# Performance work log

Measured on AMD Instinct MI355X. Metric: run time of the kernel, lower is better.

The kernel has to match this reference:

```python
import jax, jax.numpy as jnp
import numpy as np

N = 300000
GRID = 256
K = 27  # 3x3x3 kernel offsets
C = 128


def _build_neighbors(rng):
    # sample unique occupied voxels in a GRID^3 lattice (sorted linear ids)
    lin = np.unique(rng.integers(0, GRID ** 3, size=int(N * 1.3)))[:N]
    z = lin // (GRID * GRID)
    y = (lin // GRID) % GRID
    x = lin % GRID
    nbr = np.full((N, K), -1, np.int32)
    k = 0
    for dz in (-1, 0, 1):
        for dy in (-1, 0, 1):
            for dx in (-1, 0, 1):
                nz, ny, nx = z + dz, y + dy, x + dx
                valid = (nz >= 0) & (nz < GRID) & (ny >= 0) & (ny < GRID) & (nx >= 0) & (nx < GRID)
                nlin = (nz * GRID + ny) * GRID + nx
                pos = np.clip(np.searchsorted(lin, nlin), 0, N - 1)
                found = valid & (lin[pos] == nlin)
                nbr[:, k] = np.where(found, pos, -1).astype(np.int32)
                k += 1
    return nbr


def setup_inputs() -> dict:
    key = jax.random.key(0)
    ks = jax.random.split(key, 8)
    s = 0.05
    rng = np.random.default_rng(0)
    nbr_idx = jnp.asarray(_build_neighbors(rng))
    return {
        "x_feat": jnp.ones((N, 1), jnp.float32),
        "W_in": jax.random.normal(ks[0], (K, 1, C), jnp.float32) * s,
        "b_in": jnp.zeros((C,), jnp.float32),
        "W_res": jax.random.normal(ks[1], (3, 2, K, C, C), jnp.float32) * s,
        "b_res": jnp.zeros((3, 2, C), jnp.float32),
        "W_out": jax.random.normal(ks[2], (K, C, C), jnp.float32) * s,
        "b_out": jnp.zeros((C,), jnp.float32),
        "Wf1": jax.random.normal(ks[3], (C, C), jnp.float32) * s,
        "bf1": jnp.zeros((C,), jnp.float32),
        "Wf2": jax.random.normal(ks[4], (C, C), jnp.float32) * s,
        "bf2": jnp.zeros((C,), jnp.float32),
        "Wf3": jax.random.normal(ks[5], (C, 3), jnp.float32) * s,
        "bf3": jnp.zeros((3,), jnp.float32),
        "nbr_idx": nbr_idx,
    }


def _sconv(x, nbr, W, b):
    # sparse 3^3 conv: per-offset gather -> GEMM -> masked accumulate
    # x: [N,Cin], nbr: [N,K] (-1 = no neighbor), W: [K,Cin,Cout]
    Cout = W.shape[-1]
    def body(k, acc):
        idx = nbr[:, k]
        g = jnp.where((idx >= 0)[:, None], x[jnp.maximum(idx, 0)], 0.0)
        return acc + g @ W[k]
    acc = jnp.zeros((x.shape[0], Cout), x.dtype)
    return jax.lax.fori_loop(0, W.shape[0], body, acc) + b


def _decoder(x_feat, nbr, W_in, b_in, W_res, b_res, W_out, b_out, Wf1, bf1, Wf2, bf2, Wf3, bf3):
    h = jax.nn.relu(_sconv(x_feat, nbr, W_in, b_in))
    for i in range(W_res.shape[0]):  # ResNetBlock: conv-relu-conv + residual
        r = jax.nn.relu(_sconv(h, nbr, W_res[i, 0], b_res[i, 0]))
        r = _sconv(r, nbr, W_res[i, 1], b_res[i, 1])
        h = h + r
    h = _sconv(h, nbr, W_out, b_out)
    # fc stack of 1x1 convs (pointwise GEMMs)
    h = jax.nn.relu(h @ Wf1 + bf1)
    h = jax.nn.relu(h @ Wf2 + bf2)
    return h @ Wf3 + bf3  # [N,3] predicted coordinate offsets


def reference(x_feat, W_in, b_in, W_res, b_res, W_out, b_out, Wf1, bf1, Wf2, bf2, Wf3, bf3, nbr_idx):
    return _decoder(x_feat, nbr_idx, W_in, b_in, W_res, b_res, W_out, b_out, Wf1, bf1, Wf2, bf2, Wf3, bf3)
```

## Files before the change

kernel.cpp:

```cpp
#include <hip/hip_runtime.h>
#include <hip/hip_bf16.h>
#include <stdint.h>

#define NNODES 300000
#define KNBR   27
#define CDIM   128
#define P_ROWS   219968
#define MAXTILES 2048
#define MAXSLOT  16
#define NT_SELF  ((NNODES + 127) / 128)
#define TPB      4


typedef __bf16 bf16x8_t __attribute__((ext_vector_type(8)));
typedef __bf16 bf16x4_t __attribute__((ext_vector_type(4)));
typedef float  f32x4_t  __attribute__((ext_vector_type(4)));

union BP8 { bf16x8_t v; __hip_bfloat16 h[8]; };
union BP4 { bf16x4_t v; __hip_bfloat16 h[4]; };

__device__ __forceinline__ void gl2lds16(const void* g, void* l) {
  __builtin_amdgcn_global_load_lds(
      reinterpret_cast<const __attribute__((address_space(1))) uint32_t*>(
          reinterpret_cast<uintptr_t>(g)),
      reinterpret_cast<__attribute__((address_space(3))) uint32_t*>(
          reinterpret_cast<uintptr_t>(l)),
      16, 0, 0);
}

__global__ void prep_weights(const float* __restrict__ Wres,
                             const float* __restrict__ Wout,
                             const float* __restrict__ Wf1,
                             const float* __restrict__ Wf2,
                             __hip_bfloat16* __restrict__ wbf) {
  int b = blockIdx.x;
  int m = b >> 7;
  int cout = b & 127;
  int cin = threadIdx.x;
  const float* src;
  if (m < 162)      src = Wres + (size_t)m * 16384;
  else if (m < 189) src = Wout + (size_t)(m - 162) * 16384;
  else if (m == 189) src = Wf1;
  else               src = Wf2;
  float v = src[cin * 128 + cout];
  int sp = (cin & 15) * 8 + (cin >> 4);
  wbf[(size_t)m * 16384 + cout * 128 + sp] = __float2bfloat16(v);
}

__global__ void prep_bias(const float* __restrict__ b_res,
                          const float* __restrict__ b_out,
                          const float* __restrict__ bf1,
                          const float* __restrict__ bf2,
                          float* __restrict__ bp) {
  int v = blockIdx.x;
  int p = threadIdx.x;
  const float* src;
  if (v < 6)       src = b_res + v * 128;
  else if (v == 6) src = b_out;
  else if (v == 7) src = bf1;
  else             src = bf2;
  bp[v * 128 + p] = src[(p & 7) * 16 + (p >> 3)];
}

__global__ void prep_win(const float* __restrict__ Win,
                         __hip_bfloat16* __restrict__ WinT) {
  int c = threadIdx.x;
  for (int k = 0; k < 32; ++k)
    WinT[c * 32 + k] = __float2bfloat16(k < 27 ? Win[k * 128 + c] : 0.0f);
}

__global__ void init_meta(int* __restrict__ segcnt, __hip_bfloat16* __restrict__ z) {
  int t = threadIdx.x;
  if (t < 32) segcnt[t] = 0;
  if (t == 0) { segcnt[128] = 0; segcnt[129] = 0; }
  z[t] = __float2bfloat16(0.0f);
}

__global__ void count_pairs(const int* __restrict__ nbr, int* __restrict__ segcnt,
                            unsigned int* __restrict__ nmask,
                            int* __restrict__ vlist) {
  __shared__ int lc[27];
  int t = threadIdx.x;
  if (t < 27) lc[t] = 0;
  __syncthreads();
  int n = blockIdx.x * 256 + t;
  if (n < NNODES) {
    int nb[27];
    #pragma unroll
    for (int k = 0; k < 27; ++k) nb[k] = nbr[n * 27 + k];
    unsigned int mask = 0;
    #pragma unroll
    for (int k = 0; k < 27; ++k)
      if (k != 13 && nb[k] >= 0) mask |= (1u << k);
    int pc = __popc(mask);
    while (pc > MAXSLOT) {
      mask &= ~(1u << (31 - __clz((int)mask)));
      --pc;
    }
    unsigned int m = mask;
    int j = 0;
    while (m) {
      int k = __ffs(m) - 1; m &= m - 1;
      vlist[n * MAXSLOT + j] = nb[k]; ++j;
      atomicAdd(&lc[k], 1);
    }
    nmask[n] = mask;
  }
  __syncthreads();
  if (t < 27 && t != 13 && lc[t]) atomicAdd(&segcnt[t], lc[t]);
}

__global__ void scan_tiles(const int* __restrict__ segcnt,
                           int* __restrict__ segbase, int* __restrict__ seglen,
                           int* __restrict__ cursor,
                           int* __restrict__ tile_k, int* __restrict__ tile_row0,
                           int* __restrict__ tile_rows,
                           int* __restrict__ ntile) {
  __shared__ int sbase[27], slen[27], tbase[27];
  int t = threadIdx.x;
  for (int i = t; i < MAXTILES; i += 256) tile_k[i] = -1;
  if (t < 32) cursor[t] = 0;
  if (t == 0) {
    int base = 0, tb = 0;
    for (int k = 0; k < 27; ++k) {
      int c = (k == 13) ? 0 : segcnt[k];
      if (base + c > P_ROWS) c = P_ROWS - base;
      if (c < 0) c = 0;
      sbase[k] = base; slen[k] = c; tbase[k] = tb;
      base += c;
      tb += (c + 127) >> 7;
    }
    ntile[0] = tb;
  }
  __syncthreads();
  if (t < 27) {
    segbase[t] = sbase[t];
    seglen[t] = slen[t];
    if (t != 13) {
      int idx = tbase[t];
      for (int r = 0; r < slen[t]; r += 128, ++idx) {
        if (idx < MAXTILES) {
          tile_k[idx] = t;
          tile_row0[idx] = sbase[t] + r;
          tile_rows[idx] = (slen[t] - r < 128) ? (slen[t] - r) : 128;
        }
      }
    }
  }
}

__global__ void fill_pairs(const unsigned int* __restrict__ nmask,
                           const int* __restrict__ vlist,
                           const int* __restrict__ segbase, const int* __restrict__ seglen,
                           int* __restrict__ cursor,
                           int* __restrict__ pr_src, int* __restrict__ pr_dst,
                           int* __restrict__ dinfo, int* __restrict__ dcursor) {
  __shared__ int lc[27], lb[27];
  __shared__ int dloc, dbase_s;
  int t = threadIdx.x;
  if (t < 27) lc[t] = 0;
  if (t == 0) dloc = 0;
  __syncthreads();
  int n = blockIdx.x * 256 + t;
  unsigned int mask = (n < NNODES) ? nmask[n] : 0u;
  int myj = __popc(mask);
  int myoff = myj ? atomicAdd(&dloc, myj) : 0;
  unsigned int m = mask;
  while (m) { int k = __ffs(m) - 1; m &= m - 1; atomicAdd(&lc[k], 1); }
  __syncthreads();
  if (t < 27) { lb[t] = lc[t] ? atomicAdd(&cursor[t], lc[t]) : 0; lc[t] = 0; }
  if (t == 0) dbase_s = dloc ? atomicAdd(dcursor, dloc) : 0;
  __syncthreads();
  if (n < NNODES) {
    int dbase = dbase_s + myoff;
    int jj = 0, vidx = 0;
    m = mask;
    while (m) {
      int k = __ffs(m) - 1; m &= m - 1;
      int lp = atomicAdd(&lc[k], 1);
      int pos = lb[k] + lp;
      if (pos < seglen[k]) {
        int slot = segbase[k] + pos;
        pr_src[slot] = vlist[n * MAXSLOT + vidx];
        pr_dst[slot] = dbase + jj;
        ++jj;
      }
      ++vidx;
    }
    dinfo[n] = (dbase << 5) | jj;
  }
}

__global__ void build_g(const float* __restrict__ xf, const int* __restrict__ nbr,
                        __hip_bfloat16* __restrict__ G) {
  int e = blockIdx.x * 256 + threadIdx.x;
  if (e >= NNODES * 32) return;
  int n = e >> 5, j = e & 31;
  float v = 0.0f;
  if (j < 27) {
    int idx = nbr[n * 27 + j];
    if (idx >= 0) v = xf[idx];
  }
  G[e] = __float2bfloat16(v);
}

__global__ __launch_bounds__(256, 2)
void l1_gemm(const __hip_bfloat16* __restrict__ G,
             const __hip_bfloat16* __restrict__ WinT,
             const float* __restrict__ bin,
             __hip_bfloat16* __restrict__ Aout) {
  __shared__ unsigned short As[128 * 32];

  const int t    = threadIdx.x;
  const int wid  = t >> 6;
  const int lane = t & 63;
  const int quad = lane >> 4;
  const int l16  = lane & 15;
  const int m0   = blockIdx.x * 128;
  const int m_base = (wid & 1) * 64;
  const int n_base = (wid >> 1) * 64;

  bf16x8_t bfr[4];
  #pragma unroll
  for (int ni = 0; ni < 4; ++ni)
    bfr[ni] = *(const bf16x8_t*)(WinT + (n_base + ni * 16 + l16) * 32 + quad * 8);

  float bv[4];
  #pragma unroll
  for (int ni = 0; ni < 4; ++ni) bv[ni] = bin[n_base + ni * 16 + l16];

  const char* Gb = (const char*)(G + (size_t)m0 * 32);
  #pragma unroll
  for (int i = 0; i < 2; ++i) {
    int row = i * 64 + (t >> 2);
    int slot = t & 3;
    gl2lds16(Gb + (size_t)row * 64 + ((slot ^ (row & 3)) * 16),
             (char*)As + i * 4096 + t * 16);
  }
  __syncthreads();

  f32x4_t acc[4][4];
  #pragma unroll
  for (int i = 0; i < 4; ++i)
    #pragma unroll
    for (int j = 0; j < 4; ++j)
      acc[i][j] = (f32x4_t){0.f, 0.f, 0.f, 0.f};

  bf16x8_t af[4];
  #pragma unroll
  for (int mi = 0; mi < 4; ++mi)
    af[mi] = *(const bf16x8_t*)(As + (m_base + mi * 16 + l16) * 32 +
                                ((quad ^ (l16 & 3)) * 8));
  #pragma unroll
  for (int mi = 0; mi < 4; ++mi)
    #pragma unroll
    for (int ni = 0; ni < 4; ++ni)
      acc[mi][ni] = __builtin_amdgcn_mfma_f32_16x16x32_bf16(af[mi], bfr[ni], acc[mi][ni], 0, 0, 0);

  const int nb4 = n_base >> 4;
  #pragma unroll
  for (int mi = 0; mi < 4; ++mi)
    #pragma unroll
    for (int r = 0; r < 4; ++r) {
      int node = m0 + m_base + mi * 16 + quad * 4 + r;
      if (node < NNODES) {
        BP4 o;
        #pragma unroll
        for (int ni = 0; ni < 4; ++ni) {
          float v = acc[mi][ni][r] + bv[ni];
          v = v > 0.0f ? v : 0.0f;
          o.h[ni] = __float2bfloat16(v);
        }
        *(bf16x4_t*)(Aout + (size_t)node * 128 + l16 * 8 + nb4) = o.v;
      }
    }
}

__global__ __launch_bounds__(256, 2)
void pair_gemm(const __hip_bfloat16* __restrict__ Ain,
               const __hip_bfloat16* __restrict__ Wl,
               const int* __restrict__ pr_src,
               const int* __restrict__ pr_dst,
               const int* __restrict__ tile_k, const int* __restrict__ tile_row0,
               const int* __restrict__ tile_rows,
               __hip_bfloat16* __restrict__ P,
               const __hip_bfloat16* __restrict__ zrow) {
  const int t    = threadIdx.x;
  const int wid  = t >> 6;
  const int lane = t & 63;
  const int quad = lane >> 4;
  const int l16  = lane & 15;
  const int m_base = wid * 32;

  bf16x8_t bfr[8][4];
  int tk_cur = -1;

  #pragma unroll 1
  for (int it = 0; it < TPB; ++it) {
    const int tile = blockIdx.x * TPB + it;
    if (tile >= MAXTILES) break;
    const int tk = tile_k[tile];
    if (tk < 0) break;
    const int row0 = tile_row0[tile];
    const int rows = tile_rows[tile];

    if (tk != tk_cur) {
      const __hip_bfloat16* Wb = Wl + (size_t)tk * 16384;
      #pragma unroll
      for (int ni = 0; ni < 8; ++ni)
        #pragma unroll
        for (int kk = 0; kk < 4; ++kk)
          bfr[ni][kk] = *(const bf16x8_t*)(Wb + (ni * 16 + l16) * 128 + kk * 32 + quad * 8);
      tk_cur = tk;
    }

    const __hip_bfloat16* rp[2];
    #pragma unroll
    for (int mi = 0; mi < 2; ++mi) {
      int row = m_base + mi * 16 + l16;
      rp[mi] = zrow;
      if (row < rows) rp[mi] = Ain + (size_t)pr_src[row0 + row] * 128;
    }
    int dst[2][4];
    #pragma unroll
    for (int mi = 0; mi < 2; ++mi)
      #pragma unroll
      for (int r = 0; r < 4; ++r) {
        int row = m_base + mi * 16 + quad * 4 + r;
        dst[mi][r] = (row < rows) ? pr_dst[row0 + row] : -1;
      }

    f32x4_t acc[2][8];
    #pragma unroll
    for (int i = 0; i < 2; ++i)
      #pragma unroll
      for (int j = 0; j < 8; ++j)
        acc[i][j] = (f32x4_t){0.f, 0.f, 0.f, 0.f};

    #pragma unroll
    for (int kk = 0; kk < 4; ++kk) {
      bf16x8_t af[2];
      #pragma unroll
      for (int mi = 0; mi < 2; ++mi)
        af[mi] = *(const bf16x8_t*)(rp[mi] + kk * 32 + quad * 8);
      #pragma unroll
      for (int mi = 0; mi < 2; ++mi)
        #pragma unroll
        for (int ni = 0; ni < 8; ++ni)
          acc[mi][ni] = __builtin_amdgcn_mfma_f32_16x16x32_bf16(af[mi], bfr[ni][kk], acc[mi][ni], 0, 0, 0);
    }

    #pragma unroll
    for (int mi = 0; mi < 2; ++mi)
      #pragma unroll
      for (int r = 0; r < 4; ++r) {
        if (dst[mi][r] >= 0) {
          BP8 o;
          #pragma unroll
          for (int ni = 0; ni < 8; ++ni)
            o.h[ni] = __float2bfloat16(acc[mi][ni][r]);
          *(bf16x8_t*)(P + (size_t)dst[mi][r] * 128 + l16 * 8) = o.v;
        }
      }
  }
}

template <int EPI, bool HASP>
__global__ __launch_bounds__(256, 2)
void self_gemm(const __hip_bfloat16* __restrict__ Ain,
               const __hip_bfloat16* __restrict__ W13,
               const float* __restrict__ bp,
               const __hip_bfloat16* __restrict__ P,
               const int* __restrict__ dinfo,
               __hip_bfloat16* __restrict__ Aout,
               const __hip_bfloat16* __restrict__ zrow) {
  const int t    = threadIdx.x;
  const int wid  = t >> 6;
  const int lane = t & 63;
  const int quad = lane >> 4;
  const int l16  = lane & 15;
  const int m_base = wid * 32;

  bf16x8_t bfr[8][4];
  #pragma unroll
  for (int ni = 0; ni < 8; ++ni)
    #pragma unroll
    for (int kk = 0; kk < 4; ++kk)
      bfr[ni][kk] = *(const bf16x8_t*)(W13 + (ni * 16 + l16) * 128 + kk * 32 + quad * 8);

  float bb[8];
  {
    f32x4_t b0 = *(const f32x4_t*)(bp + l16 * 8);
    f32x4_t b1 = *(const f32x4_t*)(bp + l16 * 8 + 4);
    #pragma unroll
    for (int i = 0; i < 4; ++i) { bb[i] = b0[i]; bb[i + 4] = b1[i]; }
  }

  #pragma unroll 1
  for (int tile = blockIdx.x; tile < NT_SELF; tile += gridDim.x) {
    const int m0 = tile * 128;

    int dif[2][4];
    if (HASP) {
      #pragma unroll
      for (int mi = 0; mi < 2; ++mi)
        #pragma unroll
        for (int r = 0; r < 4; ++r) {
          int node = m0 + m_base + mi * 16 + quad * 4 + r;
          dif[mi][r] = (node < NNODES) ? dinfo[node] : 0;
        }
    }

    f32x4_t acc[2][8];
    #pragma unroll
    for (int i = 0; i < 2; ++i)
      #pragma unroll
      for (int j = 0; j < 8; ++j)
        acc[i][j] = (f32x4_t){0.f, 0.f, 0.f, 0.f};

    const __hip_bfloat16* Abase = Ain + (size_t)(m0 + m_base + l16) * 128;

    #pragma unroll
    for (int kk = 0; kk < 4; ++kk) {
      bf16x8_t af[2];
      #pragma unroll
      for (int mi = 0; mi < 2; ++mi)
        af[mi] = *(const bf16x8_t*)(Abase + mi * 2048 + kk * 32 + quad * 8);
      #pragma unroll
      for (int mi = 0; mi < 2; ++mi)
        #pragma unroll
        for (int ni = 0; ni < 8; ++ni)
          acc[mi][ni] = __builtin_amdgcn_mfma_f32_16x16x32_bf16(af[mi], bfr[ni][kk], acc[mi][ni], 0, 0, 0);
    }

    #pragma unroll
    for (int mi = 0; mi < 2; ++mi) {
      const int nodeb = m0 + m_base + mi * 16 + quad * 4;
      bf16x8_t hold[4], pf[4];
      int cnt4[4], base4[4];
      #pragma unroll
      for (int r = 0; r < 4; ++r) {
        int node = nodeb + r;
        bool ok = node < NNODES;
        if (EPI == 1)
          hold[r] = *(const bf16x8_t*)((ok ? Aout + (size_t)node * 128 : zrow) + l16 * 8);
        if (HASP) {
          int d = dif[mi][r];
          cnt4[r] = d & 31;
          base4[r] = d >> 5;
          pf[r] = *(const bf16x8_t*)((cnt4[r] > 0 ? P + (size_t)base4[r] * 128 : zrow) + l16 * 8);
        }
      }
      #pragma unroll
      for (int r = 0; r < 4; ++r) {
        int node = nodeb + r;
        if (node >= NNODES) continue;
        float add[8];
        #pragma unroll
        for (int ni = 0; ni < 8; ++ni) add[ni] = bb[ni];
        if (HASP) {
          if (cnt4[r] > 0) {
            #pragma unroll
            for (int ni = 0; ni < 8; ++ni) add[ni] += (float)pf[r][ni];
          }
          for (int j = 1; j < cnt4[r]; ++j) {
            bf16x8_t pv = *(const bf16x8_t*)(P + (size_t)(base4[r] + j) * 128 + l16 * 8);
            #pragma unroll
            for (int ni = 0; ni < 8; ++ni) add[ni] += (float)pv[ni];
          }
        }
        BP8 o;
        #pragma unroll
        for (int ni = 0; ni < 8; ++ni) {
          float v = acc[mi][ni][r] + add[ni];
          if (EPI == 0) {
            v = v > 0.0f ? v : 0.0f;
            o.h[ni] = __float2bfloat16(v);
          } else if (EPI == 1) {
            o.h[ni] = __float2bfloat16((float)hold[r][ni] + v);
          } else {
            o.h[ni] = __float2bfloat16(v);
          }
        }
        *(bf16x8_t*)(Aout + (size_t)node * 128 + l16 * 8) = o.v;
      }
    }
  }
}

__global__ void layer1_kernel(const float* __restrict__ xf,
                              const float* __restrict__ Win,
                              const float* __restrict__ bin,
                              const int* __restrict__ nbr,
                              __hip_bfloat16* __restrict__ abf) {
  int n = blockIdx.x;
  int c = threadIdx.x;
  float acc = bin[c];
  #pragma unroll 9
  for (int k = 0; k < KNBR; ++k) {
    int idx = nbr[n * KNBR + k];
    if (idx >= 0) acc += xf[idx] * Win[k * 128 + c];
  }
  acc = acc > 0.0f ? acc : 0.0f;
  int sp = (c & 15) * 8 + (c >> 4);
  abf[(size_t)n * 128 + sp] = __float2bfloat16(acc);
}

template <int EPI>
__global__ __launch_bounds__(256, 2)
void sconv_kernel(const __hip_bfloat16* __restrict__ Ain,
                  const __hip_bfloat16* __restrict__ Wt,
                  const float* __restrict__ bias,
                  const int* __restrict__ nbr,
                  int nk,
                  __hip_bfloat16* __restrict__ Aout,
                  const __hip_bfloat16* __restrict__ zrow) {
  __shared__ unsigned short As[128 * 128];
  __shared__ unsigned short Bs[128 * 128];

  const int t    = threadIdx.x;
  const int wid  = t >> 6;
  const int lane = t & 63;
  const int quad = lane >> 4;
  const int l16  = lane & 15;
  const int m0   = blockIdx.x * 128;

  f32x4_t acc[4][4];
  #pragma unroll
  for (int i = 0; i < 4; ++i)
    #pragma unroll
    for (int j = 0; j < 4; ++j)
      acc[i][j] = (f32x4_t){0.f, 0.f, 0.f, 0.f};

  const int m_base = (wid & 1) * 64;
  const int n_base = (wid >> 1) * 64;

  for (int k = 0; k < nk; ++k) {
    {
      const char* wsrc = (const char*)(Wt + (size_t)k * 16384);
      #pragma unroll
      for (int i = 0; i < 8; ++i) {
        uint32_t off = (uint32_t)wid * 8192 + (uint32_t)i * 1024;
        int row = wid * 32 + i * 4 + quad;
        uint32_t goff = (uint32_t)row * 256 + (uint32_t)((l16 ^ (row & 7)) * 16);
        gl2lds16(wsrc + goff, (char*)Bs + off);
      }
    }
    {
      #pragma unroll
      for (int i = 0; i < 8; ++i) {
        int r = i * 16 + wid * 4 + quad;
        int node = m0 + r;
        const __hip_bfloat16* rowp;
        if (nbr) {
          int idx = (node < NNODES) ? nbr[node * KNBR + k] : -1;
          rowp = (idx >= 0) ? (Ain + (size_t)idx * 128) : zrow;
        } else {
          rowp = (node < NNODES) ? (Ain + (size_t)node * 128) : zrow;
        }
        uint32_t ldsoff = (uint32_t)(i * 16 + wid * 4) * 256;
        gl2lds16((const char*)rowp + ((l16 ^ (r & 7)) * 16), (char*)As + ldsoff);
      }
    }
    __syncthreads();

    #pragma unroll
    for (int kk = 0; kk < 4; ++kk) {
      const int p = ((kk * 4 + quad) ^ (l16 & 7)) * 8;
      bf16x8_t af[4], bfr[4];
      #pragma unroll
      for (int mi = 0; mi < 4; ++mi)
        af[mi] = *(const bf16x8_t*)(As + (m_base + mi * 16 + l16) * 128 + p);
      #pragma unroll
      for (int ni = 0; ni < 4; ++ni)
        bfr[ni] = *(const bf16x8_t*)(Bs + (n_base + ni * 16 + l16) * 128 + p);
      #pragma unroll
      for (int mi = 0; mi < 4; ++mi)
        #pragma unroll
        for (int ni = 0; ni < 4; ++ni)
          acc[mi][ni] = __builtin_amdgcn_mfma_f32_16x16x32_bf16(af[mi], bfr[ni], acc[mi][ni], 0, 0, 0);
    }
    __syncthreads();
  }

  const int nb4 = n_base >> 4;
  #pragma unroll
  for (int ni = 0; ni < 4; ++ni) {
    int sp = l16 * 8 + nb4 + ni;
    float bvv = bias[sp];
    #pragma unroll
    for (int mi = 0; mi < 4; ++mi) {
      #pragma unroll
      for (int r = 0; r < 4; ++r) {
        int row = m_base + mi * 16 + quad * 4 + r;
        int node = m0 + row;
        if (node < NNODES) {
          float v = acc[mi][ni][r] + bvv;
          size_t o = (size_t)node * 128 + sp;
          if (EPI == 0) {
            v = v > 0.0f ? v : 0.0f;
            Aout[o] = __float2bfloat16(v);
          } else if (EPI == 1) {
            Aout[o] = __float2bfloat16(__bfloat162float(Aout[o]) + v);
          } else {
            Aout[o] = __float2bfloat16(v);
          }
        }
      }
    }
  }
}

__global__ void fc3_kernel(const __hip_bfloat16* __restrict__ r,
                           const float* __restrict__ W,
                           const float* __restrict__ b,
                           float* __restrict__ out) {
  int n = blockIdx.x * 256 + threadIdx.x;
  if (n >= NNODES) return;
  float a0 = b[0], a1 = b[1], a2 = b[2];
  const bf16x8_t* rp = (const bf16x8_t*)(r + (size_t)n * 128);
  #pragma unroll
  for (int c8 = 0; c8 < 16; ++c8) {
    bf16x8_t v8 = rp[c8];
    #pragma unroll
    for (int j = 0; j < 8; ++j) {
      float v = (float)v8[j];
      int c = j * 16 + c8;
      a0 += v * W[c * 3 + 0];
      a1 += v * W[c * 3 + 1];
      a2 += v * W[c * 3 + 2];
    }
  }
  out[n * 3 + 0] = a0;
  out[n * 3 + 1] = a1;
  out[n * 3 + 2] = a2;
}

extern "C" void kernel_launch(void* const* d_in, const int* in_sizes, int n_in,
                              void* d_out, int out_size, void* d_ws, size_t ws_size,
                              hipStream_t stream) {
  const float* x_feat = (const float*)d_in[0];
  const float* W_in   = (const float*)d_in[1];
  const float* b_in   = (const float*)d_in[2];
  const float* W_res  = (const float*)d_in[3];
  const float* b_res  = (const float*)d_in[4];
  const float* W_out  = (const float*)d_in[5];
  const float* b_out  = (const float*)d_in[6];
  const float* Wf1    = (const float*)d_in[7];
  const float* bf1    = (const float*)d_in[8];
  const float* Wf2    = (const float*)d_in[9];
  const float* bf2    = (const float*)d_in[10];
  const float* Wf3    = (const float*)d_in[11];
  const float* bf3    = (const float*)d_in[12];
  const int*   nbr    = (const int*)d_in[13];
  float* out = (float*)d_out;

  char* ws = (char*)d_ws;
  __hip_bfloat16* abf0 = (__hip_bfloat16*)ws;
  __hip_bfloat16* abf1 = (__hip_bfloat16*)(ws +  76800000);
  __hip_bfloat16* wbf  = (__hip_bfloat16*)(ws + 153600000);
  __hip_bfloat16* zrow = (__hip_bfloat16*)(ws + 159858688);
  __hip_bfloat16* P    = (__hip_bfloat16*)(ws + 159858944);
  __hip_bfloat16* WinT = (__hip_bfloat16*)(ws + 159858944 + 56320000 - 8192);
  int* pr_dst    = (int*)(ws + 216178944);
  unsigned int* nmask = (unsigned int*)(ws + 217058944);
  int* dinfo     = (int*)(ws + 235378944);
  int* pr_src    = (int*)(ws + 236578944);
  int* segcnt    = (int*)(ws + 237458944);
  int* segbase   = segcnt + 32;
  int* seglen    = segcnt + 64;
  int* cursor    = segcnt + 96;
  int* ntile     = segcnt + 128;
  int* dcursor   = segcnt + 129;
  int* tile_k    = (int*)(ws + 237463040);
  int* tile_row0 = tile_k + MAXTILES;
  int* tile_rows = tile_k + 2 * MAXTILES;
  float* bp      = (float*)(ws + 237487616);
  __hip_bfloat16* G = abf1;
  int* vlist = (int*)P;
  const size_t SPARSE_NEED = 237487616 + 4608 + 512;

  const int GB = (NNODES + 127) / 128;
  __hip_bfloat16* W0 = wbf;

  prep_weights<<<191 * 128, 128, 0, stream>>>(W_res, W_out, Wf1, Wf2, wbf);
  init_meta<<<1, 128, 0, stream>>>(segcnt, zrow);

  if (ws_size >= SPARSE_NEED) {
    prep_bias<<<9, 128, 0, stream>>>(b_res, b_out, bf1, bf2, bp);
    prep_win<<<1, 128, 0, stream>>>(W_in, WinT);
    build_g<<<(NNODES * 32 + 255) / 256, 256, 0, stream>>>(x_feat, nbr, G);
    l1_gemm<<<GB, 256, 0, stream>>>(G, WinT, b_in, abf0);

    const int CB2 = (NNODES + 255) / 256;
    count_pairs<<<CB2, 256, 0, stream>>>(nbr, segcnt, nmask, vlist);
    scan_tiles<<<1, 256, 0, stream>>>(segcnt, segbase, seglen, cursor,
                                      tile_k, tile_row0, tile_rows, ntile);
    fill_pairs<<<CB2, 256, 0, stream>>>(nmask, vlist, segbase, seglen, cursor,
                                        pr_src, pr_dst, dinfo, dcursor);

    #define CONV(IN, OUT, WLAYER, BV, EPI)                                             \
      pair_gemm<<<MAXTILES / TPB, 256, 0, stream>>>(IN, WLAYER, pr_src, pr_dst,        \
                                                    tile_k, tile_row0, tile_rows,      \
                                                    P, zrow);                          \
      self_gemm<EPI, true><<<512, 256, 0, stream>>>(IN, (WLAYER) + 13 * 16384,         \
                                                    bp + (BV) * 128, P, dinfo, OUT, zrow);

    CONV(abf0, abf1, W0 +   0 * 16384, 0, 0)
    CONV(abf1, abf0, W0 +  27 * 16384, 1, 1)
    CONV(abf0, abf1, W0 +  54 * 16384, 2, 0)
    CONV(abf1, abf0, W0 +  81 * 16384, 3, 1)
    CONV(abf0, abf1, W0 + 108 * 16384, 4, 0)
    CONV(abf1, abf0, W0 + 135 * 16384, 5, 1)
    CONV(abf0, abf1, W0 + 162 * 16384, 6, 2)
    #undef CONV

    self_gemm<0, false><<<512, 256, 0, stream>>>(abf1, W0 + 189 * 16384, bp + 7 * 128,
                                                 nullptr, nullptr, abf0, zrow);
    self_gemm<0, false><<<512, 256, 0, stream>>>(abf0, W0 + 190 * 16384, bp + 8 * 128,
                                                 nullptr, nullptr, abf1, zrow);
  } else {
    prep_bias<<<9, 128, 0, stream>>>(b_res, b_out, bf1, bf2, bp);
    layer1_kernel<<<NNODES, 128, 0, stream>>>(x_feat, W_in, b_in, nbr, abf0);
    sconv_kernel<0><<<GB, 256, 0, stream>>>(abf0, W0 +   0 * 16384, bp + 0 * 128, nbr, 27, abf1, zrow);
    sconv_kernel<1><<<GB, 256, 0, stream>>>(abf1, W0 +  27 * 16384, bp + 1 * 128, nbr, 27, abf0, zrow);
    sconv_kernel<0><<<GB, 256, 0, stream>>>(abf0, W0 +  54 * 16384, bp + 2 * 128, nbr, 27, abf1, zrow);
    sconv_kernel<1><<<GB, 256, 0, stream>>>(abf1, W0 +  81 * 16384, bp + 3 * 128, nbr, 27, abf0, zrow);
    sconv_kernel<0><<<GB, 256, 0, stream>>>(abf0, W0 + 108 * 16384, bp + 4 * 128, nbr, 27, abf1, zrow);
    sconv_kernel<1><<<GB, 256, 0, stream>>>(abf1, W0 + 135 * 16384, bp + 5 * 128, nbr, 27, abf0, zrow);
    sconv_kernel<2><<<GB, 256, 0, stream>>>(abf0, W0 + 162 * 16384, bp + 6 * 128, nbr, 27, abf1, zrow);
    sconv_kernel<0><<<GB, 256, 0, stream>>>(abf1, W0 + 189 * 16384, bp + 7 * 128, nullptr, 1, abf0, zrow);
    sconv_kernel<0><<<GB, 256, 0, stream>>>(abf0, W0 + 190 * 16384, bp + 8 * 128, nullptr, 1, abf1, zrow);
  }

  fc3_kernel<<<(NNODES + 255) / 256, 256, 0, stream>>>(abf1, Wf3, bf3, out);
}
```

Measured before the change: 973.5 us.

## Stage conv weights in swizzled LDS instead of registers to raise occupancy

Both pair_gemm and self_gemm now load the 128x128 bf16 weight tile into LDS with async global-to-LDS copies, using an XOR swizzle, and read B fragments from LDS per k-step instead of holding 128 VGPRs of weights. This frees registers so launch bounds can rise from 2 to 4 blocks per CU. pair_gemm drops its multi-tile-per-block loop and launches one block per tile, and the self_gemm grid doubles. The trade is extra LDS traffic per MFMA plus a full weight reload for every tile, which loses the previous reuse across consecutive tiles with the same offset.

```diff
diff --git a/kernel.cpp b/kernel.cpp
--- a/kernel.cpp
+++ b/kernel.cpp
@@ -9,7 +9,7 @@
 #define MAXTILES 2048
 #define MAXSLOT  16
 #define NT_SELF  ((NNODES + 127) / 128)
-#define TPB      4
+#define SELF_GRID 1024
 
 
 typedef __bf16 bf16x8_t __attribute__((ext_vector_type(8)));
@@ -276,7 +276,7 @@
     }
 }
 
-__global__ __launch_bounds__(256, 2)
+__global__ __launch_bounds__(256, 4)
 void pair_gemm(const __hip_bfloat16* __restrict__ Ain,
                const __hip_bfloat16* __restrict__ Wl,
                const int* __restrict__ pr_src,
@@ -285,6 +285,13 @@
                const int* __restrict__ tile_rows,
                __hip_bfloat16* __restrict__ P,
                const __hip_bfloat16* __restrict__ zrow) {
+  __shared__ unsigned short Ws[128 * 128];
+
+  const int tk = tile_k[blockIdx.x];
+  if (tk < 0) return;
+  const int row0 = tile_row0[blockIdx.x];
+  const int rows = tile_rows[blockIdx.x];
+
   const int t    = threadIdx.x;
   const int wid  = t >> 6;
   const int lane = t & 63;
@@ -292,81 +299,73 @@
   const int l16  = lane & 15;
   const int m_base = wid * 32;
 
-  bf16x8_t bfr[8][4];
-  int tk_cur = -1;
-
-  #pragma unroll 1
-  for (int it = 0; it < TPB; ++it) {
-    const int tile = blockIdx.x * TPB + it;
-    if (tile >= MAXTILES) break;
-    const int tk = tile_k[tile];
-    if (tk < 0) break;
-    const int row0 = tile_row0[tile];
-    const int rows = tile_rows[tile];
-
-    if (tk != tk_cur) {
-      const __hip_bfloat16* Wb = Wl + (size_t)tk * 16384;
-      #pragma unroll
-      for (int ni = 0; ni < 8; ++ni)
-        #pragma unroll
-        for (int kk = 0; kk < 4; ++kk)
-          bfr[ni][kk] = *(const bf16x8_t*)(Wb + (ni * 16 + l16) * 128 + kk * 32 + quad * 8);
-      tk_cur = tk;
-    }
-
-    const __hip_bfloat16* rp[2];
-    #pragma unroll
-    for (int mi = 0; mi < 2; ++mi) {
-      int row = m_base + mi * 16 + l16;
-      rp[mi] = zrow;
-      if (row < rows) rp[mi] = Ain + (size_t)pr_src[row0 + row] * 128;
-    }
-    int dst[2][4];
+  {
+    const char* wsrc = (const char*)(Wl + (size_t)tk * 16384);
+    #pragma unroll
+    for (int i = 0; i < 8; ++i) {
+      int row = wid * 32 + i * 4 + quad;
+      gl2lds16(wsrc + (uint32_t)row * 256 + (uint32_t)((l16 ^ (row & 7)) * 16),
+               (char*)Ws + wid * 8192 + i * 1024 + lane * 16);
+    }
+  }
+
+  const __hip_bfloat16* rp[2];
+  #pragma unroll
+  for (int mi = 0; mi < 2; ++mi) {
+    int row = m_base + mi * 16 + l16;
+    rp[mi] = zrow;
+    if (row < rows) rp[mi] = Ain + (size_t)pr_src[row0 + row] * 128;
+  }
+  int dst[2][4];
+  #pragma unroll
+  for (int mi = 0; mi < 2; ++mi)
+    #pragma unroll
+    for (int r = 0; r < 4; ++r) {
+      int row = m_base + mi * 16 + quad * 4 + r;
+      dst[mi][r] = (row < rows) ? pr_dst[row0 + row] : -1;
+    }
+
+  __syncthreads();
+
+  f32x4_t acc[2][8];
+  #pragma unroll
+  for (int i = 0; i < 2; ++i)
+    #pragma unroll
+    for (int j = 0; j < 8; ++j)
+      acc[i][j] = (f32x4_t){0.f, 0.f, 0.f, 0.f};
+
+  #pragma unroll
+  for (int kk = 0; kk < 4; ++kk) {
+    bf16x8_t af[2];
     #pragma unroll
     for (int mi = 0; mi < 2; ++mi)
-      #pragma unroll
-      for (int r = 0; r < 4; ++r) {
-        int row = m_base + mi * 16 + quad * 4 + r;
-        dst[mi][r] = (row < rows) ? pr_dst[row0 + row] : -1;
-      }
-
-    f32x4_t acc[2][8];
-    #pragma unroll
-    for (int i = 0; i < 2; ++i)
-      #pragma unroll
-      for (int j = 0; j < 8; ++j)
-        acc[i][j] = (f32x4_t){0.f, 0.f, 0.f, 0.f};
-
-    #pragma unroll
-    for (int kk = 0; kk < 4; ++kk) {
-      bf16x8_t af[2];
+      af[mi] = *(const bf16x8_t*)(rp[mi] + kk * 32 + quad * 8);
+    #pragma unroll
+    for (int ni = 0; ni < 8; ++ni) {
+      bf16x8_t bw = *(const bf16x8_t*)(Ws + (ni * 16 + l16) * 128 +
+                                       (((kk * 4 + quad) ^ (l16 & 7)) * 8));
       #pragma unroll
       for (int mi = 0; mi < 2; ++mi)
-        af[mi] = *(const bf16x8_t*)(rp[mi] + kk * 32 + quad * 8);
-      #pragma unroll
-      for (int mi = 0; mi < 2; ++mi)
+        acc[mi][ni] = __builtin_amdgcn_mfma_f32_16x16x32_bf16(af[mi], bw, acc[mi][ni], 0, 0, 0);
+    }
+  }
+
+  #pragma unroll
+  for (int mi = 0; mi < 2; ++mi)
+    #pragma unroll
+    for (int r = 0; r < 4; ++r) {
+      if (dst[mi][r] >= 0) {
+        BP8 o;
         #pragma unroll
         for (int ni = 0; ni < 8; ++ni)
-          acc[mi][ni] = __builtin_amdgcn_mfma_f32_16x16x32_bf16(af[mi], bfr[ni][kk], acc[mi][ni], 0, 0, 0);
-    }
-
-    #pragma unroll
-    for (int mi = 0; mi < 2; ++mi)
-      #pragma unroll
-      for (int r = 0; r < 4; ++r) {
-        if (dst[mi][r] >= 0) {
-          BP8 o;
-          #pragma unroll
-          for (int ni = 0; ni < 8; ++ni)
-            o.h[ni] = __float2bfloat16(acc[mi][ni][r]);
-          *(bf16x8_t*)(P + (size_t)dst[mi][r] * 128 + l16 * 8) = o.v;
-        }
-      }
-  }
+          o.h[ni] = __float2bfloat16(acc[mi][ni][r]);
+        *(bf16x8_t*)(P + (size_t)dst[mi][r] * 128 + l16 * 8) = o.v;
+      }
+    }
 }
 
 template <int EPI, bool HASP>
-__global__ __launch_bounds__(256, 2)
+__global__ __launch_bounds__(256, 4)
 void self_gemm(const __hip_bfloat16* __restrict__ Ain,
                const __hip_bfloat16* __restrict__ W13,
                const float* __restrict__ bp,
@@ -374,6 +373,8 @@
                const int* __restrict__ dinfo,
                __hip_bfloat16* __restrict__ Aout,
                const __hip_bfloat16* __restrict__ zrow) {
+  __shared__ unsigned short Ws[128 * 128];
+
   const int t    = threadIdx.x;
   const int wid  = t >> 6;
   const int lane = t & 63;
@@ -381,12 +382,15 @@
   const int l16  = lane & 15;
   const int m_base = wid * 32;
 
-  bf16x8_t bfr[8][4];
-  #pragma unroll
-  for (int ni = 0; ni < 8; ++ni)
-    #pragma unroll
-    for (int kk = 0; kk < 4; ++kk)
-      bfr[ni][kk] = *(const bf16x8_t*)(W13 + (ni * 16 + l16) * 128 + kk * 32 + quad * 8);
+  {
+    const char* wsrc = (const char*)W13;
+    #pragma unroll
+    for (int i = 0; i < 8; ++i) {
+      int row = wid * 32 + i * 4 + quad;
+      gl2lds16(wsrc + (uint32_t)row * 256 + (uint32_t)((l16 ^ (row & 7)) * 16),
+               (char*)Ws + wid * 8192 + i * 1024 + lane * 16);
+    }
+  }
 
   float bb[8];
   {
@@ -395,6 +399,8 @@
     #pragma unroll
     for (int i = 0; i < 4; ++i) { bb[i] = b0[i]; bb[i + 4] = b1[i]; }
   }
+
+  __syncthreads();
 
   #pragma unroll 1
   for (int tile = blockIdx.x; tile < NT_SELF; tile += gridDim.x) {
@@ -427,10 +433,13 @@
       for (int mi = 0; mi < 2; ++mi)
         af[mi] = *(const bf16x8_t*)(Abase + mi * 2048 + kk * 32 + quad * 8);
       #pragma unroll
-      for (int mi = 0; mi < 2; ++mi)
+      for (int ni = 0; ni < 8; ++ni) {
+        bf16x8_t bw = *(const bf16x8_t*)(Ws + (ni * 16 + l16) * 128 +
+                                         (((kk * 4 + quad) ^ (l16 & 7)) * 8));
         #pragma unroll
-        for (int ni = 0; ni < 8; ++ni)
-          acc[mi][ni] = __builtin_amdgcn_mfma_f32_16x16x32_bf16(af[mi], bfr[ni][kk], acc[mi][ni], 0, 0, 0);
+        for (int mi = 0; mi < 2; ++mi)
+          acc[mi][ni] = __builtin_amdgcn_mfma_f32_16x16x32_bf16(af[mi], bw, acc[mi][ni], 0, 0, 0);
+      }
     }
 
     #pragma unroll
@@ -700,11 +709,12 @@
                                         pr_src, pr_dst, dinfo, dcursor);
 
     #define CONV(IN, OUT, WLAYER, BV, EPI)                                             \
-      pair_gemm<<<MAXTILES / TPB, 256, 0, stream>>>(IN, WLAYER, pr_src, pr_dst,        \
-                                                    tile_k, tile_row0, tile_rows,      \
-                                                    P, zrow);                          \
-      self_gemm<EPI, true><<<512, 256, 0, stream>>>(IN, (WLAYER) + 13 * 16384,         \
-                                                    bp + (BV) * 128, P, dinfo, OUT, zrow);
+      pair_gemm<<<MAXTILES, 256, 0, stream>>>(IN, WLAYER, pr_src, pr_dst,              \
+                                              tile_k, tile_row0, tile_rows,            \
+                                              P, zrow);                                \
+      self_gemm<EPI, true><<<SELF_GRID, 256, 0, stream>>>(IN, (WLAYER) + 13 * 16384,   \
+                                                          bp + (BV) * 128, P, dinfo,   \
+                                                          OUT, zrow);
 
     CONV(abf0, abf1, W0 +   0 * 16384, 0, 0)
     CONV(abf1, abf0, W0 +  27 * 16384, 1, 1)
@@ -715,10 +725,10 @@
     CONV(abf0, abf1, W0 + 162 * 16384, 6, 2)
     #undef CONV
 
-    self_gemm<0, false><<<512, 256, 0, stream>>>(abf1, W0 + 189 * 16384, bp + 7 * 128,
-                                                 nullptr, nullptr, abf0, zrow);
-    self_gemm<0, false><<<512, 256, 0, stream>>>(abf0, W0 + 190 * 16384, bp + 8 * 128,
-                                                 nullptr, nullptr, abf1, zrow);
+    self_gemm<0, false><<<SELF_GRID, 256, 0, stream>>>(abf1, W0 + 189 * 16384, bp + 7 * 128,
+                                                       nullptr, nullptr, abf0, zrow);
+    self_gemm<0, false><<<SELF_GRID, 256, 0, stream>>>(abf0, W0 + 190 * 16384, bp + 8 * 128,
+                                                       nullptr, nullptr, abf1, zrow);
   } else {
     prep_bias<<<9, 128, 0, stream>>>(b_res, b_out, bf1, bf2, bp);
     layer1_kernel<<<NNODES, 128, 0, stream>>>(x_feat, W_in, b_in, nbr, abf0);
```

After: 1.948 ms. +100.2%, slower.
